# Optimization experiments

Hardware: AMD Instinct MI355X
Metric: run time of the kernel (lower is better)

The kernel has to match this reference:

```python
import jax, jax.numpy as jnp
import numpy as np

B, LQ, LK, D, H = 4, 1024, 1024, 512, 8


def setup_inputs() -> dict:
    key = jax.random.key(0)
    ks = jax.random.split(key, 6)
    # xavier_normal for (D, D): std = sqrt(2 / (D + D))
    std_qkv = (2.0 / (D + D)) ** 0.5
    std_p = (2.0 / (H * D + D)) ** 0.5
    x = jax.random.normal(ks[0], (B, LQ, D), dtype=jnp.float32)
    states = jax.random.normal(ks[1], (B, LK, D), dtype=jnp.float32)
    mask = jnp.ones((B, LQ, LK), dtype=jnp.int32)
    # per-head full-size QKV weights, stacked over heads: [H, D, D]
    Wq = jax.random.normal(ks[2], (H, D, D), dtype=jnp.float32) * std_qkv
    Wk = jax.random.normal(ks[3], (H, D, D), dtype=jnp.float32) * std_qkv
    Wv = jax.random.normal(ks[4], (H, D, D), dtype=jnp.float32) * std_qkv
    Wp = jax.random.normal(ks[5], (D, H * D), dtype=jnp.float32) * std_p
    return {"x": x, "states": states, "mask": mask,
            "Wq": Wq, "Wk": Wk, "Wv": Wv, "Wp": Wp}


def reference(x, states, mask, Wq, Wk, Wv, Wp):
    # Per-head linear projections (nn.Linear: y = x @ W.T), batched over heads.
    q = jnp.einsum('bld,hed->bhle', x, Wq)        # [B,H,Lq,D]
    k = jnp.einsum('bsd,hed->bhse', states, Wk)   # [B,H,Lk,D]
    v = jnp.einsum('bsd,hed->bhse', states, Wv)   # [B,H,Lk,D]
    scale = 1.0 / (D ** 0.5)
    scores = jnp.einsum('bhle,bhse->bhls', q, k) * scale  # [B,H,Lq,Lk]
    scores = jnp.where(mask[:, None, :, :] == 0, -jnp.inf, scores)
    attn = jax.nn.softmax(scores, axis=-1)
    # Original does broadcast multiply + sum; mathematically this is attn @ v.
    ctx = jnp.einsum('bhls,bhse->bhle', attn, v)  # [B,H,Lq,D]
    # torch.cat over heads in order -> head-major last dim
    ctx = jnp.transpose(ctx, (0, 2, 1, 3)).reshape(B, LQ, H * D)
    return ctx @ Wp.T  # [B,Lq,D]
```

## Files before the change

### kernel.cpp

```cpp
#include <hip/hip_runtime.h>
#include <hip/hip_bf16.h>
#include <cstdint>
#include <cstddef>


typedef __bf16 bf16;
typedef __bf16 bf16x4 __attribute__((ext_vector_type(4)));
typedef __bf16 bf16x8 __attribute__((ext_vector_type(8)));
typedef float f32x4 __attribute__((ext_vector_type(4)));

__device__ inline void gload_lds16(const void* g, void* l) {
  __builtin_amdgcn_global_load_lds(
      (const __attribute__((address_space(1))) void*)g,
      (__attribute__((address_space(3))) void*)l, 16, 0, 0);
}

template <typename CT, int MODE>
__device__ __forceinline__ void gemm_body(
    bf16* As, bf16* Bs,
    const bf16* __restrict__ A, const bf16* __restrict__ B, CT* __restrict__ C,
    int K, int lda, int ldb, int ldc, int m0, int n0, float scale,
    const unsigned* __restrict__ mrow, float* __restrict__ sumrow)
{
  const int t = threadIdx.x;
  const int lane = t & 63, w = t >> 6;
  const int wm = w >> 1, wn = w & 1;

  const int srow = t >> 3;
  const int schunk = (t & 7) ^ (srow & 7);
  const bf16* Ag = A + (size_t)(m0 + srow) * lda + schunk * 8;
  const bf16* Bg = B + (size_t)(n0 + srow) * ldb + schunk * 8;
  bf16* Als = As + t * 8;
  bf16* Bls = Bs + t * 8;

  f32x4 acc[4][4] = {};
  const int rr = lane & 15;
  const int q4 = lane >> 4;

  const int kIters = K >> 6;
  for (int kt = 0; kt < kIters; ++kt) {
    __syncthreads();
#pragma unroll
    for (int i = 0; i < 4; ++i) {
      gload_lds16(Ag + (size_t)(32 * i) * lda, Als + i * 2048);
      gload_lds16(Bg + (size_t)(32 * i) * ldb, Bls + i * 2048);
    }
    Ag += 64; Bg += 64;
    __syncthreads();

#pragma unroll
    for (int kk = 0; kk < 2; ++kk) {
      bf16x8 af[4], bfr[4];
      const int ck = kk * 4 + q4;
#pragma unroll
      for (int r = 0; r < 4; ++r) {
        const int R = wm * 64 + r * 16 + rr;
        af[r] = *(const bf16x8*)(As + R * 64 + ((ck ^ (R & 7)) << 3));
      }
#pragma unroll
      for (int c = 0; c < 4; ++c) {
        const int R = wn * 64 + c * 16 + rr;
        bfr[c] = *(const bf16x8*)(Bs + R * 64 + ((ck ^ (R & 7)) << 3));
      }
#pragma unroll
      for (int r = 0; r < 4; ++r)
#pragma unroll
        for (int c = 0; c < 4; ++c)
          acc[r][c] = __builtin_amdgcn_mfma_f32_16x16x32_bf16(af[r], bfr[c], acc[r][c], 0, 0, 0);
    }
  }

  if (MODE == 0) {
#pragma unroll
    for (int r = 0; r < 4; ++r) {
#pragma unroll
      for (int c = 0; c < 4; ++c) {
        const int gr0 = m0 + wm * 64 + r * 16 + (q4 << 2);
        const int gc = n0 + wn * 64 + c * 16 + rr;
#pragma unroll
        for (int i = 0; i < 4; ++i)
          C[(size_t)(gr0 + i) * ldc + gc] = (CT)(acc[r][c][i] * scale);
      }
    }
  } else {
    const int cb0 = (n0 + wn * 64) >> 5;
#pragma unroll
    for (int r = 0; r < 4; ++r) {
#pragma unroll
      for (int i = 0; i < 4; ++i) {
        const int row = m0 + wm * 64 + r * 16 + (q4 << 2) + i;
        const unsigned mw0 = mrow[(row << 5) + cb0];
        const unsigned mw1 = mrow[(row << 5) + cb0 + 1];
        float ps = 0.0f;
#pragma unroll
        for (int c = 0; c < 4; ++c) {
          const int gc = n0 + wn * 64 + c * 16 + rr;
          const unsigned mw = (c >= 2) ? mw1 : mw0;
          const unsigned bit = (mw >> (((c & 1) << 4) + rr)) & 1u;
          float p = bit ? __expf(acc[r][c][i] * scale) : 0.0f;
          C[(size_t)row * ldc + gc] = (CT)p;
          ps += p;
        }
        ps += __shfl_xor(ps, 1); ps += __shfl_xor(ps, 2);
        ps += __shfl_xor(ps, 4); ps += __shfl_xor(ps, 8);
        if (rr == 0) atomicAdd(sumrow + row, ps);
      }
    }
  }
}

__global__ __launch_bounds__(256) void prep_kernel(
    const float* __restrict__ x, const float* __restrict__ st,
    const float* __restrict__ Wq, const float* __restrict__ Wk,
    const float* __restrict__ Wp, const float* __restrict__ Wv,
    const int* __restrict__ mask,
    bf16* __restrict__ xb, bf16* __restrict__ stb, bf16* __restrict__ wqb,
    bf16* __restrict__ wkb, bf16* __restrict__ wpb, bf16* __restrict__ WvT,
    unsigned* __restrict__ mbits, float* __restrict__ sums)
{
  const int lin = blockIdx.x;
  const int t = threadIdx.x;
  if (lin < 10240) {
    const float* s; bf16* d;
    switch (lin >> 11) {
      case 0: s = x; d = xb; break;
      case 1: s = st; d = stb; break;
      case 2: s = Wq; d = wqb; break;
      case 3: s = Wk; d = wkb; break;
      default: s = Wp; d = wpb; break;
    }
    const int i = ((lin & 2047) * 256 + t) * 4;
    float4 v = *(const float4*)(s + i);
    bf16x4 o;
    o[0] = (bf16)v.x; o[1] = (bf16)v.y; o[2] = (bf16)v.z; o[3] = (bf16)v.w;
    *(bf16x4*)(d + i) = o;
  } else if (lin < 12288) {
    const int gid = (lin - 10240) * 256 + t;
    const int e0 = (gid & 127) * 4;
    const int d = (gid >> 7) & 511;
    const int h = gid >> 16;
    const float* src = Wv + (size_t)h * 262144 + (size_t)e0 * 512 + d;
    bf16x4 o;
    o[0] = (bf16)src[0];
    o[1] = (bf16)src[512];
    o[2] = (bf16)src[1024];
    o[3] = (bf16)src[1536];
    *(bf16x4*)(WvT + (size_t)h * 262144 + (size_t)d * 512 + e0) = o;
  } else if (lin < 12800) {
    const int gid = (lin - 12288) * 256 + t;
    const int* src = mask + (size_t)gid * 32;
    unsigned bits = 0;
#pragma unroll
    for (int j = 0; j < 32; j += 4) {
      int4 v = *(const int4*)(src + j);
      if (v.x) bits |= 1u << j;
      if (v.y) bits |= 1u << (j + 1);
      if (v.z) bits |= 1u << (j + 2);
      if (v.w) bits |= 1u << (j + 3);
    }
    mbits[gid] = bits;
  } else {
    const int i = ((lin - 12800) * 256 + t) * 4;
    *(float4*)(sums + i) = make_float4(0.f, 0.f, 0.f, 0.f);
  }
}

__global__ __launch_bounds__(256) void proj_kernel(
    const bf16* __restrict__ xb, const bf16* __restrict__ stb,
    const bf16* __restrict__ wqb, const bf16* __restrict__ wkb,
    const bf16* __restrict__ wpb, const bf16* __restrict__ WvT,
    bf16* __restrict__ q, bf16* __restrict__ k, bf16* __restrict__ U)
{
  __shared__ bf16 As[128 * 64];
  __shared__ bf16 Bs[128 * 64];
  const int lin = blockIdx.x;
  if (lin < 2048) {
    const int g = ((lin >> 8) << 3) | (lin & 7);
    const int tile = (lin >> 3) & 31;
    const int job = g >> 5;
    const int zz = g & 31;
    const size_t zb = zz >> 3, zh = zz & 7;
    const bf16* Ain = (job == 0) ? xb : stb;
    const bf16* W = (job == 0) ? wqb : wkb;
    bf16* Cout = (job == 0) ? q : k;
    gemm_body<bf16, 0>(As, Bs, Ain + zb * 524288, W + zh * 262144,
        Cout + zb * 4194304 + zh * 524288, 512, 512, 512, 512,
        (tile >> 2) * 128, (tile & 3) * 128, 1.0f, nullptr, nullptr);
  } else {
    const int lin2 = lin - 2048;
    const int h = lin2 >> 4;
    const int tile = lin2 & 15;
    gemm_body<bf16, 0>(As, Bs, wpb + (size_t)h * 512, WvT + (size_t)h * 262144,
        U + (size_t)h * 262144, 512, 4096, 512, 512,
        (tile >> 2) * 128, (tile & 3) * 128, 1.0f, nullptr, nullptr);
  }
}

__global__ __launch_bounds__(256) void big_kernel(
    const bf16* __restrict__ q, const bf16* __restrict__ k,
    const bf16* __restrict__ U, const bf16* __restrict__ stb,
    bf16* __restrict__ P, bf16* __restrict__ VWT,
    const unsigned* __restrict__ mbits, float* __restrict__ sums, float scale)
{
  __shared__ bf16 As[128 * 64];
  __shared__ bf16 Bs[128 * 64];
  const int lin = blockIdx.x;
  if (lin < 2048) {
    const int z = ((lin >> 9) << 3) | (lin & 7);
    const int j = (lin >> 3) & 63;
    const int zb = z >> 3, zh = z & 7;
    const bf16* A = q + (size_t)zb * 4194304 + (size_t)zh * 524288;
    const bf16* B = k + (size_t)zb * 4194304 + (size_t)zh * 524288;
    bf16* C = P + (size_t)zb * 8388608 + (size_t)zh * 1048576;
    const unsigned* mrow = mbits + ((size_t)zb << 15);
    float* sumrow = sums + ((size_t)z << 10);
    gemm_body<bf16, 1>(As, Bs, A, B, C, 512, 512, 512, 1024,
                       (j >> 3) * 128, (j & 7) * 128, scale, mrow, sumrow);
  } else {
    const int lin2 = lin - 2048;
    const int z = ((lin2 >> 8) << 3) | (lin2 & 7);
    const int j = (lin2 >> 3) & 31;
    const int zb = z >> 3, zh = z & 7;
    gemm_body<bf16, 0>(As, Bs, U + (size_t)zh * 262144, stb + (size_t)zb * 524288,
        VWT + (size_t)zb * 4194304 + (size_t)zh * 524288, 512, 512, 512, 1024,
        (j >> 3) * 128, (j & 7) * 128, 1.0f, nullptr, nullptr);
  }
}

__global__ __launch_bounds__(256) void pvw_kernel(
    const bf16* __restrict__ P, const bf16* __restrict__ VWT,
    const float* __restrict__ sums, float* __restrict__ out)
{
  __shared__ bf16 As[128 * 64];
  __shared__ bf16 Bs[128 * 64];
  const int lin = blockIdx.x;
  const int z = ((lin >> 8) << 3) | (lin & 7);
  const int j = (lin >> 3) & 31;
  const int zb = z >> 2, hp = z & 3;
  const int m0 = (j >> 2) * 128, n0 = (j & 3) * 128;
  const int t = threadIdx.x;
  const int lane = t & 63, w = t >> 6;
  const int wm = w >> 1, wn = w & 1;
  const int srow = t >> 3, schunk = (t & 7) ^ (srow & 7);
  const int rr = lane & 15, q4 = lane >> 4;
  bf16* Als = As + t * 8;
  bf16* Bls = Bs + t * 8;

  f32x4 accO[4][4] = {};

#pragma unroll
  for (int hh = 0; hh < 2; ++hh) {
    const int h = hp * 2 + hh;
    const bf16* Ag = P + (size_t)zb * 8388608 + (size_t)h * 1048576
                       + (size_t)(m0 + srow) * 1024 + schunk * 8;
    const bf16* Bg = VWT + (size_t)zb * 4194304 + (size_t)h * 524288
                        + (size_t)(n0 + srow) * 1024 + schunk * 8;
    f32x4 acc[4][4] = {};
    for (int kt = 0; kt < 16; ++kt) {
      __syncthreads();
#pragma unroll
      for (int i = 0; i < 4; ++i) {
        gload_lds16(Ag + (size_t)(32 * i) * 1024, Als + i * 2048);
        gload_lds16(Bg + (size_t)(32 * i) * 1024, Bls + i * 2048);
      }
      Ag += 64; Bg += 64;
      __syncthreads();
#pragma unroll
      for (int kk = 0; kk < 2; ++kk) {
        bf16x8 af[4], bfr[4];
        const int ck = kk * 4 + q4;
#pragma unroll
        for (int r = 0; r < 4; ++r) {
          const int R = wm * 64 + r * 16 + rr;
          af[r] = *(const bf16x8*)(As + R * 64 + ((ck ^ (R & 7)) << 3));
        }
#pragma unroll
        for (int c = 0; c < 4; ++c) {
          const int R = wn * 64 + c * 16 + rr;
          bfr[c] = *(const bf16x8*)(Bs + R * 64 + ((ck ^ (R & 7)) << 3));
        }
#pragma unroll
        for (int r = 0; r < 4; ++r)
#pragma unroll
          for (int c = 0; c < 4; ++c)
            acc[r][c] = __builtin_amdgcn_mfma_f32_16x16x32_bf16(af[r], bfr[c], acc[r][c], 0, 0, 0);
      }
    }
    const float* srs = sums + ((size_t)zb * 8 + h) * 1024;
#pragma unroll
    for (int r = 0; r < 4; ++r) {
#pragma unroll
      for (int i = 0; i < 4; ++i) {
        const float inv = 1.0f / srs[m0 + wm * 64 + r * 16 + (q4 << 2) + i];
#pragma unroll
        for (int c = 0; c < 4; ++c)
          accO[r][c][i] += acc[r][c][i] * inv;
      }
    }
  }

  float* Cp = out + (size_t)zb * 524288;
#pragma unroll
  for (int r = 0; r < 4; ++r) {
#pragma unroll
    for (int c = 0; c < 4; ++c) {
      const int gr0 = m0 + wm * 64 + r * 16 + (q4 << 2);
      const int gc = n0 + wn * 64 + c * 16 + rr;
#pragma unroll
      for (int i = 0; i < 4; ++i)
        atomicAdd(Cp + (size_t)(gr0 + i) * 512 + gc, accO[r][c][i]);
    }
  }
}

extern "C" void kernel_launch(void* const* d_in, const int* in_sizes, int n_in,
                              void* d_out, int out_size, void* d_ws, size_t ws_size,
                              hipStream_t stream) {
  const float* x    = (const float*)d_in[0];
  const float* st   = (const float*)d_in[1];
  const int*   mask = (const int*)d_in[2];
  const float* Wq   = (const float*)d_in[3];
  const float* Wk   = (const float*)d_in[4];
  const float* Wv   = (const float*)d_in[5];
  const float* Wp   = (const float*)d_in[6];
  float* out = (float*)d_out;

  char* ws = (char*)d_ws;
  const size_t MB = 1048576;
  bf16* xb  = (bf16*)(ws);
  bf16* stb = (bf16*)(ws + 4 * MB);
  bf16* wqb = (bf16*)(ws + 8 * MB);
  bf16* wkb = (bf16*)(ws + 12 * MB);
  bf16* wpb = (bf16*)(ws + 16 * MB);
  bf16* WvT = (bf16*)(ws + 20 * MB);
  bf16* U   = (bf16*)(ws + 24 * MB);
  bf16* q   = (bf16*)(ws + 28 * MB);
  bf16* k   = (bf16*)(ws + 60 * MB);
  bf16* VWT = (bf16*)(ws + 92 * MB);
  bf16* sc  = (bf16*)(ws + 124 * MB);
  unsigned* mbits = (unsigned*)(ws + 188 * MB);
  float*    sums  = (float*)(ws + 189 * MB);

  dim3 blk(256);
  const float scale = 0.04419417382415922f;

  hipMemsetAsync(d_out, 0, (size_t)out_size * sizeof(float), stream);

  prep_kernel<<<dim3(12832), blk, 0, stream>>>(x, st, Wq, Wk, Wp, Wv, mask,
      xb, stb, wqb, wkb, wpb, WvT, mbits, sums);

  proj_kernel<<<dim3(2176), blk, 0, stream>>>(xb, stb, wqb, wkb, wpb, WvT,
      q, k, U);

  big_kernel<<<dim3(3072), blk, 0, stream>>>(q, k, U, stb, sc, VWT,
      mbits, sums, scale);

  pvw_kernel<<<dim3(512), blk, 0, stream>>>(sc, VWT, sums, out);
}
```

Measured before the change: 298.4 us.

## Split PV-Wp GEMM per head into bf16 partials with separate reduction

The final P·(VWp) kernel used to loop over two heads per block and accumulate into the output with float atomics after a memset. Now each block handles a single head, doubling the grid to 1024 blocks, and writes normalized bf16 partial results into a per-head buffer that reuses the q workspace region. A new reduce8 kernel sums the eight head partials into the fp32 output, replacing both the atomics and the memset. This trades atomic contention and low occupancy for an extra launch, an extra round trip through the partial buffer, and bf16 rounding of each partial.

```diff
diff --git a/kernel.cpp b/kernel.cpp
--- a/kernel.cpp
+++ b/kernel.cpp
@@ -229,14 +229,14 @@
 
 __global__ __launch_bounds__(256) void pvw_kernel(
     const bf16* __restrict__ P, const bf16* __restrict__ VWT,
-    const float* __restrict__ sums, float* __restrict__ out)
+    const float* __restrict__ sums, bf16* __restrict__ part8)
 {
   __shared__ bf16 As[128 * 64];
   __shared__ bf16 Bs[128 * 64];
   const int lin = blockIdx.x;
   const int z = ((lin >> 8) << 3) | (lin & 7);
   const int j = (lin >> 3) & 31;
-  const int zb = z >> 2, hp = z & 3;
+  const int zb = z >> 3, zh = z & 7;
   const int m0 = (j >> 2) * 128, n0 = (j & 3) * 128;
   const int t = threadIdx.x;
   const int lane = t & 63, w = t >> 6;
@@ -246,71 +246,71 @@
   bf16* Als = As + t * 8;
   bf16* Bls = Bs + t * 8;
 
-  f32x4 accO[4][4] = {};
-
-#pragma unroll
-  for (int hh = 0; hh < 2; ++hh) {
-    const int h = hp * 2 + hh;
-    const bf16* Ag = P + (size_t)zb * 8388608 + (size_t)h * 1048576
-                       + (size_t)(m0 + srow) * 1024 + schunk * 8;
-    const bf16* Bg = VWT + (size_t)zb * 4194304 + (size_t)h * 524288
-                        + (size_t)(n0 + srow) * 1024 + schunk * 8;
-    f32x4 acc[4][4] = {};
-    for (int kt = 0; kt < 16; ++kt) {
-      __syncthreads();
-#pragma unroll
-      for (int i = 0; i < 4; ++i) {
-        gload_lds16(Ag + (size_t)(32 * i) * 1024, Als + i * 2048);
-        gload_lds16(Bg + (size_t)(32 * i) * 1024, Bls + i * 2048);
-      }
-      Ag += 64; Bg += 64;
-      __syncthreads();
-#pragma unroll
-      for (int kk = 0; kk < 2; ++kk) {
-        bf16x8 af[4], bfr[4];
-        const int ck = kk * 4 + q4;
-#pragma unroll
-        for (int r = 0; r < 4; ++r) {
-          const int R = wm * 64 + r * 16 + rr;
-          af[r] = *(const bf16x8*)(As + R * 64 + ((ck ^ (R & 7)) << 3));
-        }
-#pragma unroll
-        for (int c = 0; c < 4; ++c) {
-          const int R = wn * 64 + c * 16 + rr;
-          bfr[c] = *(const bf16x8*)(Bs + R * 64 + ((ck ^ (R & 7)) << 3));
-        }
-#pragma unroll
-        for (int r = 0; r < 4; ++r)
-#pragma unroll
-          for (int c = 0; c < 4; ++c)
-            acc[r][c] = __builtin_amdgcn_mfma_f32_16x16x32_bf16(af[r], bfr[c], acc[r][c], 0, 0, 0);
-      }
-    }
-    const float* srs = sums + ((size_t)zb * 8 + h) * 1024;
-#pragma unroll
-    for (int r = 0; r < 4; ++r) {
-#pragma unroll
-      for (int i = 0; i < 4; ++i) {
-        const float inv = 1.0f / srs[m0 + wm * 64 + r * 16 + (q4 << 2) + i];
+  const bf16* Ag = P + (size_t)zb * 8388608 + (size_t)zh * 1048576
+                     + (size_t)(m0 + srow) * 1024 + schunk * 8;
+  const bf16* Bg = VWT + (size_t)zb * 4194304 + (size_t)zh * 524288
+                      + (size_t)(n0 + srow) * 1024 + schunk * 8;
+  f32x4 acc[4][4] = {};
+  for (int kt = 0; kt < 16; ++kt) {
+    __syncthreads();
+#pragma unroll
+    for (int i = 0; i < 4; ++i) {
+      gload_lds16(Ag + (size_t)(32 * i) * 1024, Als + i * 2048);
+      gload_lds16(Bg + (size_t)(32 * i) * 1024, Bls + i * 2048);
+    }
+    Ag += 64; Bg += 64;
+    __syncthreads();
+#pragma unroll
+    for (int kk = 0; kk < 2; ++kk) {
+      bf16x8 af[4], bfr[4];
+      const int ck = kk * 4 + q4;
+#pragma unroll
+      for (int r = 0; r < 4; ++r) {
+        const int R = wm * 64 + r * 16 + rr;
+        af[r] = *(const bf16x8*)(As + R * 64 + ((ck ^ (R & 7)) << 3));
+      }
+#pragma unroll
+      for (int c = 0; c < 4; ++c) {
+        const int R = wn * 64 + c * 16 + rr;
+        bfr[c] = *(const bf16x8*)(Bs + R * 64 + ((ck ^ (R & 7)) << 3));
+      }
+#pragma unroll
+      for (int r = 0; r < 4; ++r)
 #pragma unroll
         for (int c = 0; c < 4; ++c)
-          accO[r][c][i] += acc[r][c][i] * inv;
-      }
-    }
-  }
-
-  float* Cp = out + (size_t)zb * 524288;
+          acc[r][c] = __builtin_amdgcn_mfma_f32_16x16x32_bf16(af[r], bfr[c], acc[r][c], 0, 0, 0);
+    }
+  }
+
+  const float* srs = sums + ((size_t)z << 10);
+  bf16* Cp = part8 + (size_t)zh * 2097152 + (size_t)zb * 524288;
 #pragma unroll
   for (int r = 0; r < 4; ++r) {
 #pragma unroll
-    for (int c = 0; c < 4; ++c) {
-      const int gr0 = m0 + wm * 64 + r * 16 + (q4 << 2);
-      const int gc = n0 + wn * 64 + c * 16 + rr;
-#pragma unroll
-      for (int i = 0; i < 4; ++i)
-        atomicAdd(Cp + (size_t)(gr0 + i) * 512 + gc, accO[r][c][i]);
-    }
-  }
+    for (int i = 0; i < 4; ++i) {
+      const int gr = m0 + wm * 64 + r * 16 + (q4 << 2) + i;
+      const float inv = 1.0f / srs[gr];
+#pragma unroll
+      for (int c = 0; c < 4; ++c) {
+        const int gc = n0 + wn * 64 + c * 16 + rr;
+        Cp[(size_t)gr * 512 + gc] = (bf16)(acc[r][c][i] * inv);
+      }
+    }
+  }
+}
+
+__global__ __launch_bounds__(256) void reduce8(
+    const bf16* __restrict__ part8, float* __restrict__ out)
+{
+  const size_t i = ((size_t)blockIdx.x * 256 + threadIdx.x) * 4;
+  float4 o = make_float4(0.f, 0.f, 0.f, 0.f);
+#pragma unroll
+  for (int s = 0; s < 8; ++s) {
+    bf16x4 v = *(const bf16x4*)(part8 + (size_t)s * 2097152 + i);
+    o.x += (float)v[0]; o.y += (float)v[1];
+    o.z += (float)v[2]; o.w += (float)v[3];
+  }
+  *(float4*)(out + i) = o;
 }
 
 extern "C" void kernel_launch(void* const* d_in, const int* in_sizes, int n_in,
@@ -337,23 +337,24 @@
   bf16* q   = (bf16*)(ws + 28 * MB);
   bf16* k   = (bf16*)(ws + 60 * MB);
   bf16* VWT = (bf16*)(ws + 92 * MB);
-  bf16* sc  = (bf16*)(ws + 124 * MB);
+  bf16* P   = (bf16*)(ws + 124 * MB);
   unsigned* mbits = (unsigned*)(ws + 188 * MB);
   float*    sums  = (float*)(ws + 189 * MB);
+  bf16*     part8 = (bf16*)(ws + 28 * MB);
 
   dim3 blk(256);
   const float scale = 0.04419417382415922f;
 
-  hipMemsetAsync(d_out, 0, (size_t)out_size * sizeof(float), stream);
-
   prep_kernel<<<dim3(12832), blk, 0, stream>>>(x, st, Wq, Wk, Wp, Wv, mask,
       xb, stb, wqb, wkb, wpb, WvT, mbits, sums);
 
   proj_kernel<<<dim3(2176), blk, 0, stream>>>(xb, stb, wqb, wkb, wpb, WvT,
       q, k, U);
 
-  big_kernel<<<dim3(3072), blk, 0, stream>>>(q, k, U, stb, sc, VWT,
+  big_kernel<<<dim3(3072), blk, 0, stream>>>(q, k, U, stb, P, VWT,
       mbits, sums, scale);
 
-  pvw_kernel<<<dim3(512), blk, 0, stream>>>(sc, VWT, sums, out);
-}
+  pvw_kernel<<<dim3(1024), blk, 0, stream>>>(P, VWT, sums, part8);
+
+  reduce8<<<dim3(2048), blk, 0, stream>>>(part8, out);
+}
```

After: 288.8 us. -3.2%, faster.
